# Performance work log

Measured on AMD Instinct MI355X. Metric: run time of the kernel, lower is better.

Reference implementation:

```python
import jax, jax.numpy as jnp
import numpy as np

# ---- static config ----
H, W = 60, 60
WS = 7          # window size (square)
SS = 3          # shift size
DIM = 256
NH = 8
HD = DIM // NH
N = WS * WS     # tokens per window = 49
HP = (H // WS + 1) * WS  # 63 (padded, matches __init__ mask construction)
WP = (W // WS + 1) * WS  # 63
NW = (HP // WS) * (WP // WS)  # 81 windows
EPS = 1e-5


def _rel_pos_index():
    coords = np.stack(np.meshgrid(np.arange(WS), np.arange(WS), indexing='ij'))  # (2,WS,WS)
    cf = coords.reshape(2, -1)                      # (2, N)
    rel = cf[:, :, None] - cf[:, None, :]           # (2, N, N)
    rel = rel.transpose(1, 2, 0).astype(np.int64)   # (N, N, 2)
    rel[..., 0] += WS - 1
    rel[..., 1] += WS - 1
    rel[..., 0] *= 2 * WS - 1
    return rel.sum(-1)                              # (N, N) in [0, 169)


def _attn_mask():
    img = np.zeros((HP, WP), dtype=np.float32)
    cnt = 0
    for hs in (slice(0, -WS), slice(-WS, -SS), slice(-SS, None)):
        for ws_ in (slice(0, -WS), slice(-WS, -SS), slice(-SS, None)):
            img[hs, ws_] = cnt
            cnt += 1
    mw = img.reshape(HP // WS, WS, WP // WS, WS).transpose(0, 2, 1, 3).reshape(-1, N)  # (NW, N)
    diff = mw[:, None, :] - mw[:, :, None]          # (NW, N, N)
    return np.where(diff != 0, -100.0, 0.0).astype(np.float32)


REL_IDX = _rel_pos_index()
ATTN_MASK = _attn_mask()


def layer_norm(x, g, b):
    mu = jnp.mean(x, axis=-1, keepdims=True)
    var = jnp.mean(jnp.square(x - mu), axis=-1, keepdims=True)
    return (x - mu) * jax.lax.rsqrt(var + EPS) * g + b


def setup_inputs() -> dict:
    key = jax.random.key(0)
    ks = jax.random.split(key, 8)
    B = 24
    std = 0.02
    return {
        'x': jax.random.normal(ks[0], (B, H * W, DIM), jnp.float32),
        'g1': jnp.ones((DIM,), jnp.float32),
        'b1': jnp.zeros((DIM,), jnp.float32),
        'w_qkv': jax.random.normal(ks[1], (DIM, 3 * DIM), jnp.float32) * std,
        'b_qkv': jnp.zeros((3 * DIM,), jnp.float32),
        'rel_bias_table': jax.random.normal(ks[2], ((2 * WS - 1) ** 2, NH), jnp.float32) * std,
        'w_proj': jax.random.normal(ks[3], (DIM, DIM), jnp.float32) * std,
        'b_proj': jnp.zeros((DIM,), jnp.float32),
        'g2': jnp.ones((DIM,), jnp.float32),
        'b2': jnp.zeros((DIM,), jnp.float32),
        'w_fc1': jax.random.normal(ks[4], (DIM, 4 * DIM), jnp.float32) * std,
        'b_fc1': jnp.zeros((4 * DIM,), jnp.float32),
        'w_fc2': jax.random.normal(ks[5], (4 * DIM, DIM), jnp.float32) * std,
        'b_fc2': jnp.zeros((DIM,), jnp.float32),
    }


def _swin_block(x, g1, b1, w_qkv, b_qkv, rel_bias_table, w_proj, b_proj,
                g2, b2, w_fc1, b_fc1, w_fc2, b_fc2):
    B, L, C = x.shape
    shortcut = x
    x = layer_norm(x, g1, b1).reshape(B, H, W, C)
    # pad to (HP, WP)
    x = jnp.pad(x, ((0, 0), (0, HP - H), (0, WP - W), (0, 0)))
    # cyclic shift
    x = jnp.roll(x, (-SS, -SS), axis=(1, 2))
    # window partition -> (B*NW, N, C)
    xw = x.reshape(B, HP // WS, WS, WP // WS, WS, C).transpose(0, 1, 3, 2, 4, 5)
    xw = xw.reshape(B * NW, N, C)
    # attention
    qkv = (xw @ w_qkv + b_qkv).reshape(B * NW, N, 3, NH, HD).transpose(2, 0, 3, 1, 4)
    q, k, v = qkv[0], qkv[1], qkv[2]            # (B*NW, NH, N, HD)
    q = q * (HD ** -0.5)
    attn = jnp.einsum('whnd,whmd->whnm', q, k)  # (B*NW, NH, N, N)
    rel_bias = rel_bias_table[jnp.asarray(REL_IDX)]          # (N, N, NH)
    attn = attn + rel_bias.transpose(2, 0, 1)[None]
    mask = jnp.asarray(ATTN_MASK)                            # (NW, N, N)
    attn = attn.reshape(B, NW, NH, N, N) + mask[None, :, None]
    attn = jax.nn.softmax(attn.reshape(B * NW, NH, N, N), axis=-1)
    out = jnp.einsum('whnm,whmd->whnd', attn, v)             # (B*NW, NH, N, HD)
    out = out.transpose(0, 2, 1, 3).reshape(B * NW, N, C)
    out = out @ w_proj + b_proj
    # window reverse -> (B, HP, WP, C)
    out = out.reshape(B, HP // WS, WP // WS, WS, WS, C).transpose(0, 1, 3, 2, 4, 5)
    out = out.reshape(B, HP, WP, C)
    # reverse shift, unpad
    out = jnp.roll(out, (SS, SS), axis=(1, 2))[:, :H, :W, :].reshape(B, L, C)
    x = shortcut + out
    # MLP
    y = layer_norm(x, g2, b2)
    y = jax.nn.gelu(y @ w_fc1 + b_fc1, approximate=False) @ w_fc2 + b_fc2
    return x + y


def reference(x, g1, b1, w_qkv, b_qkv, rel_bias_table, w_proj, b_proj,
              g2, b2, w_fc1, b_fc1, w_fc2, b_fc2):
    return _swin_block(x, g1, b1, w_qkv, b_qkv, rel_bias_table, w_proj, b_proj,
                       g2, b2, w_fc1, b_fc1, w_fc2, b_fc2)
```

## Files before the change

### kernel.cpp

```cpp
#include <hip/hip_runtime.h>
#include <hip/hip_bf16.h>
#include <math.h>


typedef _Float16 half8 __attribute__((ext_vector_type(8)));
typedef _Float16 half4_t __attribute__((ext_vector_type(4)));
typedef float f32x4 __attribute__((ext_vector_type(4)));

#define GLDS16(gp, lp)                                                    \
  __builtin_amdgcn_global_load_lds(                                      \
      (__attribute__((address_space(1))) const void*)(gp),               \
      (__attribute__((address_space(3))) void*)(lp), 16, 0, 0)

__device__ __forceinline__ float wave_reduce_sum(float v) {
  v += __shfl_xor(v, 1);
  v += __shfl_xor(v, 2);
  v += __shfl_xor(v, 4);
  v += __shfl_xor(v, 8);
  v += __shfl_xor(v, 16);
  v += __shfl_xor(v, 32);
  return v;
}

__global__ __launch_bounds__(256) void prep_weights(
    const float* __restrict__ wqkv, const float* __restrict__ wproj,
    const float* __restrict__ wfc1, const float* __restrict__ wfc2,
    _Float16* __restrict__ oqkv, _Float16* __restrict__ oproj,
    _Float16* __restrict__ ofc1, _Float16* __restrict__ ofc2)
{
  int idx = blockIdx.x * 256 + threadIdx.x;
  if (idx < 196608) {
    int n = idx / 256, k = idx % 256;
    oqkv[idx] = (_Float16)wqkv[k * 768 + n];
  } else if (idx < 262144) {
    int i = idx - 196608; int n = i / 256, k = i % 256;
    oproj[i] = (_Float16)wproj[k * 256 + n];
  } else if (idx < 524288) {
    int i = idx - 262144; int n = i / 256, k = i % 256;
    ofc1[i] = (_Float16)wfc1[k * 1024 + n];
  } else {
    int i = idx - 524288; int n = i / 1024, k = i % 1024;
    ofc2[i] = (_Float16)wfc2[k * 256 + n];
  }
}

__global__ __launch_bounds__(256) void prep_cb(
    const float* __restrict__ rbt, _Float16* __restrict__ cbt)
{
  int idx = blockIdx.x * 256 + threadIdx.x;
  int m = idx & 63, n = (idx >> 6) & 63;
  int hc = idx >> 12; int h = hc & 7, c = hc >> 3;
  float v;
  if (n < 49 && m < 49) {
    int i1 = n / 7, j1 = n % 7, i2 = m / 7, j2 = m % 7;
    float bias = rbt[((i1 - i2 + 6) * 13 + (j1 - j2 + 6)) * 8 + h];
    int rh1 = (c & 2) ? (i1 < 4 ? 1 : 2) : 0;
    int rh2 = (c & 2) ? (i2 < 4 ? 1 : 2) : 0;
    int rw1 = (c & 1) ? (j1 < 4 ? 1 : 2) : 0;
    int rw2 = (c & 1) ? (j2 < 4 ? 1 : 2) : 0;
    v = bias + (((rh1 != rh2) || (rw1 != rw2)) ? -100.f : 0.f);
  } else {
    v = -60000.f;
  }
  cbt[idx] = (_Float16)v;
}

__global__ __launch_bounds__(256) void ln1_window_kernel(
    const float* __restrict__ x, const float* __restrict__ g,
    const float* __restrict__ bta, _Float16* __restrict__ xw,
    int row0, int rows_c)
{
  int lrow = blockIdx.x * 4 + (threadIdx.x >> 6);
  if (lrow >= rows_c) return;
  int row = row0 + lrow;
  int lane = threadIdx.x & 63;
  int bw = row / 49, n = row - bw * 49;
  int b = bw / 81, win = bw - b * 81;
  int wh = win / 9, ww = win - wh * 9;
  int i = n / 7, j = n - i * 7;
  int sh = wh * 7 + i + 3; if (sh >= 63) sh -= 63;
  int sw = ww * 7 + j + 3; if (sw >= 63) sw -= 63;
  bool valid = (sh < 60) && (sw < 60);
  float4 v = make_float4(0.f, 0.f, 0.f, 0.f);
  if (valid)
    v = reinterpret_cast<const float4*>(x + ((size_t)b * 3600 + sh * 60 + sw) * 256)[lane];
  float s = v.x + v.y + v.z + v.w;
  s = wave_reduce_sum(s);
  float mu = s * (1.f / 256.f);
  float dx = v.x - mu, dy = v.y - mu, dz = v.z - mu, dw = v.w - mu;
  float q = dx * dx + dy * dy + dz * dz + dw * dw;
  q = wave_reduce_sum(q);
  float rs = rsqrtf(q * (1.f / 256.f) + 1e-5f);
  float4 gv = reinterpret_cast<const float4*>(g)[lane];
  float4 bv = reinterpret_cast<const float4*>(bta)[lane];
  union { _Float16 h[4]; uint2 u; } pk;
  if (valid) {
    pk.h[0] = (_Float16)(dx * rs * gv.x + bv.x);
    pk.h[1] = (_Float16)(dy * rs * gv.y + bv.y);
    pk.h[2] = (_Float16)(dz * rs * gv.z + bv.z);
    pk.h[3] = (_Float16)(dw * rs * gv.w + bv.w);
  } else {
    pk.h[0] = pk.h[1] = pk.h[2] = pk.h[3] = (_Float16)0.f;
  }
  *reinterpret_cast<uint2*>(xw + (size_t)lrow * 256 + lane * 4) = pk.u;
}

__global__ __launch_bounds__(256) void ln2_kernel(
    const float* __restrict__ xin, const float* __restrict__ g,
    const float* __restrict__ bta, _Float16* __restrict__ y)
{
  int row = blockIdx.x * 4 + (threadIdx.x >> 6);
  int lane = threadIdx.x & 63;
  float4 v = reinterpret_cast<const float4*>(xin + (size_t)row * 256)[lane];
  float s = v.x + v.y + v.z + v.w;
  s = wave_reduce_sum(s);
  float mu = s * (1.f / 256.f);
  float dx = v.x - mu, dy = v.y - mu, dz = v.z - mu, dw = v.w - mu;
  float q = dx * dx + dy * dy + dz * dz + dw * dw;
  q = wave_reduce_sum(q);
  float rs = rsqrtf(q * (1.f / 256.f) + 1e-5f);
  float4 gv = reinterpret_cast<const float4*>(g)[lane];
  float4 bv = reinterpret_cast<const float4*>(bta)[lane];
  union { _Float16 h[4]; uint2 u; } pk;
  pk.h[0] = (_Float16)(dx * rs * gv.x + bv.x);
  pk.h[1] = (_Float16)(dy * rs * gv.y + bv.y);
  pk.h[2] = (_Float16)(dz * rs * gv.z + bv.z);
  pk.h[3] = (_Float16)(dw * rs * gv.w + bv.w);
  *reinterpret_cast<uint2*>(y + (size_t)row * 256 + lane * 4) = pk.u;
}

__global__ __launch_bounds__(256, 2) void gemm_kernel(
    const _Float16* __restrict__ A, const _Float16* __restrict__ Bt,
    const float* __restrict__ bias, const float* __restrict__ resid,
    void* __restrict__ out, int M, int N, int K, int mode, int row0)
{
  __shared__ __align__(16) _Float16 lds[2][2][8192];
  const int tid = threadIdx.x;
  const int n0 = blockIdx.x * 128, m0 = blockIdx.y * 128;
  const int wv = tid >> 6, ln = tid & 63;
  const int wm = (wv >> 1) * 64, wn = (wv & 1) * 64;
  const int quad = ln >> 4, l16 = ln & 15;

  const int rl = ln >> 3;
  const int gseg = ((ln & 7) ^ rl) << 3;
  const _Float16* gA[4]; const _Float16* gB[4];
#pragma unroll
  for (int s = 0; s < 4; s++) {
    int r = wv * 32 + s * 8 + rl;
    int gm = m0 + r; if (gm >= M) gm = M - 1;
    gA[s] = A + (size_t)gm * K + gseg;
    gB[s] = Bt + (size_t)(n0 + r) * K + gseg;
  }

  int offA[2][4], offB[2][4];
#pragma unroll
  for (int i = 0; i < 4; i++) {
    int ra = wm + i * 16 + l16;
    int rb = wn + i * 16 + l16;
    int sw0 = l16 & 7;
#pragma unroll
    for (int ks = 0; ks < 2; ks++) {
      offA[ks][i] = ra * 64 + (((ks * 4 + quad) ^ sw0) << 3);
      offB[ks][i] = rb * 64 + (((ks * 4 + quad) ^ sw0) << 3);
    }
  }

  f32x4 acc[4][4];
#pragma unroll
  for (int i = 0; i < 4; i++)
#pragma unroll
    for (int j = 0; j < 4; j++) acc[i][j] = (f32x4)0.f;

#define STAGE(buf, koff)                                                   \
  {                                                                        \
    _Float16* la = &lds[buf][0][wv * 2048];                                \
    _Float16* lb = &lds[buf][1][wv * 2048];                                \
    GLDS16(gA[0] + (koff), la);        GLDS16(gB[0] + (koff), lb);         \
    GLDS16(gA[1] + (koff), la + 512);  GLDS16(gB[1] + (koff), lb + 512);   \
    GLDS16(gA[2] + (koff), la + 1024); GLDS16(gB[2] + (koff), lb + 1024);  \
    GLDS16(gA[3] + (koff), la + 1536); GLDS16(gB[3] + (koff), lb + 1536);  \
  }

  const int nt = K >> 6;
  STAGE(0, 0);
  __syncthreads();
  for (int t = 0; t < nt; t++) {
    const int cur = t & 1;
    half8 a0[4], b0[4], a1[4], b1[4];
#pragma unroll
    for (int i = 0; i < 4; i++) {
      a0[i] = *reinterpret_cast<const half8*>(&lds[cur][0][offA[0][i]]);
      a1[i] = *reinterpret_cast<const half8*>(&lds[cur][0][offA[1][i]]);
      b0[i] = *reinterpret_cast<const half8*>(&lds[cur][1][offB[0][i]]);
      b1[i] = *reinterpret_cast<const half8*>(&lds[cur][1][offB[1][i]]);
    }
    if (t + 1 < nt) STAGE(cur ^ 1, (t + 1) << 6);
#pragma unroll
    for (int i = 0; i < 4; i++)
#pragma unroll
      for (int j = 0; j < 4; j++)
        acc[i][j] = __builtin_amdgcn_mfma_f32_16x16x32_f16(b0[j], a0[i], acc[i][j], 0, 0, 0);
#pragma unroll
    for (int i = 0; i < 4; i++)
#pragma unroll
      for (int j = 0; j < 4; j++)
        acc[i][j] = __builtin_amdgcn_mfma_f32_16x16x32_f16(b1[j], a1[i], acc[i][j], 0, 0, 0);
    __syncthreads();
  }
#undef STAGE

  f32x4 bias4[4];
#pragma unroll
  for (int j = 0; j < 4; j++)
    bias4[j] = *reinterpret_cast<const f32x4*>(bias + n0 + wn + j * 16 + quad * 4);

#pragma unroll
  for (int i = 0; i < 4; i++) {
    int gm = m0 + wm + i * 16 + l16;
    if (gm >= M) continue;
    if (mode == 0) {
      _Float16* op = reinterpret_cast<_Float16*>(out) + (size_t)gm * N + n0 + wn;
#pragma unroll
      for (int j = 0; j < 4; j++) {
        float sc = (n0 + wn + j * 16) < 256 ? 0.17677669529663687f : 1.f;
        half4_t o4;
#pragma unroll
        for (int r = 0; r < 4; r++)
          o4[r] = (_Float16)((acc[i][j][r] + bias4[j][r]) * sc);
        *reinterpret_cast<half4_t*>(op + j * 16 + quad * 4) = o4;
      }
    } else if (mode == 2) {
      _Float16* op = reinterpret_cast<_Float16*>(out) + (size_t)gm * N + n0 + wn;
#pragma unroll
      for (int j = 0; j < 4; j++) {
        half4_t o4;
#pragma unroll
        for (int r = 0; r < 4; r++) {
          float v = acc[i][j][r] + bias4[j][r];
          v = 0.5f * v * (1.f + erff(v * 0.70710678118654752f));
          o4[r] = (_Float16)v;
        }
        *reinterpret_cast<half4_t*>(op + j * 16 + quad * 4) = o4;
      }
    } else if (mode == 3) {
      float* op = reinterpret_cast<float*>(out) + (size_t)gm * N + n0 + wn;
      const float* rp = resid + (size_t)gm * N + n0 + wn;
#pragma unroll
      for (int j = 0; j < 4; j++) {
        f32x4 rv = *reinterpret_cast<const f32x4*>(rp + j * 16 + quad * 4);
        f32x4 v = acc[i][j] + bias4[j] + rv;
        *reinterpret_cast<f32x4*>(op + j * 16 + quad * 4) = v;
      }
    } else {
      int gmg = gm + row0;
      int bw = gmg / 49, nn = gmg - bw * 49;
      int bidx = bw / 81, win = bw - bidx * 81;
      int wh = win / 9, wwn = win - wh * 9;
      int ii = nn / 7, jj = nn - ii * 7;
      int sh = wh * 7 + ii + 3; if (sh >= 63) sh -= 63;
      int sw = wwn * 7 + jj + 3; if (sw >= 63) sw -= 63;
      if (sh < 60 && sw < 60) {
        size_t o = ((size_t)bidx * 3600 + sh * 60 + sw) * 256 + n0 + wn;
        float* op = reinterpret_cast<float*>(out) + o;
        const float* rp = resid + o;
#pragma unroll
        for (int j = 0; j < 4; j++) {
          f32x4 rv = *reinterpret_cast<const f32x4*>(rp + j * 16 + quad * 4);
          f32x4 v = acc[i][j] + bias4[j] + rv;
          *reinterpret_cast<f32x4*>(op + j * 16 + quad * 4) = v;
        }
      }
    }
  }
}

__global__ __launch_bounds__(64) void attn_mfma(
    const _Float16* __restrict__ qkv, const _Float16* __restrict__ cbt,
    _Float16* __restrict__ outp)
{
  __shared__ __align__(16) _Float16 VT[32][72];
  __shared__ __align__(16) _Float16 Ps[64][72];
  const int bwh = blockIdx.x;
  const int bw = bwh >> 3, h = bwh & 7;
  const int win = bw % 81;
  const int wh = win / 9, ww = win - wh * 9;
  const int cls = ((wh == 8) ? 2 : 0) | ((ww == 8) ? 1 : 0);
  const int lane = threadIdx.x;
  const int quad = lane >> 4, l16 = lane & 15;

  for (int e = lane; e < 480; e += 64) {
    int d = e / 15, m = 49 + e % 15;
    VT[d][m] = (_Float16)0.f;
  }
  const size_t vbase = (size_t)bw * 49 * 768 + 512 + h * 32;
  for (int e = lane; e < 1568; e += 64) {
    int m = e >> 5, d = e & 31;
    VT[d][m] = qkv[vbase + (size_t)m * 768 + d];
  }

  const _Float16* qb = qkv + (size_t)bw * 49 * 768 + h * 32 + quad * 8;
  half8 kf[4], qf[4];
  const half8 hz = (half8)(_Float16)0.f;
#pragma unroll
  for (int t = 0; t < 4; t++) {
    int row = t * 16 + l16;
    int rc = row < 49 ? row : 48;
    half8 kv = *reinterpret_cast<const half8*>(qb + 256 + (size_t)rc * 768);
    half8 qv = *reinterpret_cast<const half8*>(qb + (size_t)rc * 768);
    kf[t] = row < 49 ? kv : hz;
    qf[t] = row < 49 ? qv : hz;
  }

  f32x4 S[4][4];
#pragma unroll
  for (int mt = 0; mt < 4; mt++)
#pragma unroll
    for (int nt = 0; nt < 4; nt++) S[mt][nt] = (f32x4)0.f;
#pragma unroll
  for (int mt = 0; mt < 4; mt++)
#pragma unroll
    for (int nt = 0; nt < 4; nt++)
      S[mt][nt] = __builtin_amdgcn_mfma_f32_16x16x32_f16(kf[mt], qf[nt], S[mt][nt], 0, 0, 0);

  const _Float16* cbp = cbt + (((size_t)cls * 8 + h) << 12);
#pragma unroll
  for (int nt = 0; nt < 4; nt++) {
    int n = nt * 16 + l16;
#pragma unroll
    for (int mt = 0; mt < 4; mt++) {
      half4_t cb4 = *reinterpret_cast<const half4_t*>(cbp + n * 64 + mt * 16 + quad * 4);
#pragma unroll
      for (int r = 0; r < 4; r++) S[mt][nt][r] += (float)cb4[r];
    }
  }

  float inv[4];
#pragma unroll
  for (int nt = 0; nt < 4; nt++) {
    float mx = -3.0e38f;
#pragma unroll
    for (int mt = 0; mt < 4; mt++)
#pragma unroll
      for (int r = 0; r < 4; r++) mx = fmaxf(mx, S[mt][nt][r]);
    mx = fmaxf(mx, __shfl_xor(mx, 16));
    mx = fmaxf(mx, __shfl_xor(mx, 32));
    float sm = 0.f;
#pragma unroll
    for (int mt = 0; mt < 4; mt++)
#pragma unroll
      for (int r = 0; r < 4; r++) {
        float e = __expf(S[mt][nt][r] - mx);
        S[mt][nt][r] = e;
        sm += e;
      }
    sm += __shfl_xor(sm, 16);
    sm += __shfl_xor(sm, 32);
    inv[nt] = 1.f / sm;
  }

#pragma unroll
  for (int nt = 0; nt < 4; nt++) {
#pragma unroll
    for (int mt = 0; mt < 4; mt++) {
      half4_t p;
#pragma unroll
      for (int r = 0; r < 4; r++) p[r] = (_Float16)(S[mt][nt][r] * inv[nt]);
      *reinterpret_cast<half4_t*>(&Ps[nt * 16 + l16][mt * 16 + quad * 4]) = p;
    }
  }
  __syncthreads();

  f32x4 O[2][4];
#pragma unroll
  for (int dt = 0; dt < 2; dt++)
#pragma unroll
    for (int nt = 0; nt < 4; nt++) O[dt][nt] = (f32x4)0.f;
#pragma unroll
  for (int ks = 0; ks < 2; ks++) {
    half8 va[2], pb[4];
#pragma unroll
    for (int dt = 0; dt < 2; dt++)
      va[dt] = *reinterpret_cast<const half8*>(&VT[dt * 16 + l16][ks * 32 + quad * 8]);
#pragma unroll
    for (int nt = 0; nt < 4; nt++)
      pb[nt] = *reinterpret_cast<const half8*>(&Ps[nt * 16 + l16][ks * 32 + quad * 8]);
#pragma unroll
    for (int dt = 0; dt < 2; dt++)
#pragma unroll
      for (int nt = 0; nt < 4; nt++)
        O[dt][nt] = __builtin_amdgcn_mfma_f32_16x16x32_f16(va[dt], pb[nt], O[dt][nt], 0, 0, 0);
  }

#pragma unroll
  for (int nt = 0; nt < 4; nt++) {
    int n = nt * 16 + l16;
    if (n < 49) {
#pragma unroll
      for (int dt = 0; dt < 2; dt++) {
        half4_t o4;
#pragma unroll
        for (int r = 0; r < 4; r++) o4[r] = (_Float16)O[dt][nt][r];
        *reinterpret_cast<half4_t*>(
            outp + ((size_t)bw * 49 + n) * 256 + h * 32 + dt * 16 + quad * 4) = o4;
      }
    }
  }
}

extern "C" void kernel_launch(void* const* d_in, const int* in_sizes, int n_in,
                              void* d_out, int out_size, void* d_ws, size_t ws_size,
                              hipStream_t stream) {
  const float* x      = (const float*)d_in[0];
  const float* g1     = (const float*)d_in[1];
  const float* b1     = (const float*)d_in[2];
  const float* w_qkv  = (const float*)d_in[3];
  const float* b_qkv  = (const float*)d_in[4];
  const float* rbt    = (const float*)d_in[5];
  const float* w_proj = (const float*)d_in[6];
  const float* b_proj = (const float*)d_in[7];
  const float* g2     = (const float*)d_in[8];
  const float* b2     = (const float*)d_in[9];
  const float* w_fc1  = (const float*)d_in[10];
  const float* b_fc1  = (const float*)d_in[11];
  const float* w_fc2  = (const float*)d_in[12];
  const float* b_fc2  = (const float*)d_in[13];
  float* outp = (float*)d_out;

  char* ws = (char*)d_ws;
  _Float16* wqkvT  = (_Float16*)(ws + 0);
  _Float16* wprojT = (_Float16*)(ws + 393216);
  _Float16* wfc1T  = (_Float16*)(ws + 524288);
  _Float16* wfc2T  = (_Float16*)(ws + 1048576);
  _Float16* cbt    = (_Float16*)(ws + 1572864);
  const size_t WB = 1835008;

  const int cand[8] = {24, 12, 8, 6, 4, 3, 2, 1};
  int cb = 1;
  for (int ci = 0; ci < 8; ci++) {
    size_t need = WB + (size_t)cand[ci] * (2032128u + 7372800u);
    if (ws_size >= need) { cb = cand[ci]; break; }
  }
  const int nch = 24 / cb;

  _Float16* r1 = (_Float16*)(ws + WB);
  _Float16* r2 = (_Float16*)(ws + WB + (size_t)cb * 2032128u);

  prep_weights<<<3072, 256, 0, stream>>>(w_qkv, w_proj, w_fc1, w_fc2,
                                         wqkvT, wprojT, wfc1T, wfc2T);
  prep_cb<<<512, 256, 0, stream>>>(rbt, cbt);

  for (int c = 0; c < nch; c++) {
    const int b0 = c * cb;
    const int rows_att = cb * 81 * 49;
    const int row0_att = b0 * 81 * 49;
    const int rows_mlp = cb * 3600;
    const int row0_mlp = b0 * 3600;

    ln1_window_kernel<<<(rows_att + 3) / 4, 256, 0, stream>>>(
        x, g1, b1, r1, row0_att, rows_att);
    {
      dim3 g(6, (rows_att + 127) / 128);
      gemm_kernel<<<g, 256, 0, stream>>>(r1, wqkvT, b_qkv, nullptr, r2,
                                         rows_att, 768, 256, 0, 0);
    }
    attn_mfma<<<cb * 81 * 8, 64, 0, stream>>>(r2, cbt, r1);
    {
      dim3 g(2, (rows_att + 127) / 128);
      gemm_kernel<<<g, 256, 0, stream>>>(r1, wprojT, b_proj, x, outp,
                                         rows_att, 256, 256, 1, row0_att);
    }
    ln2_kernel<<<rows_mlp / 4, 256, 0, stream>>>(
        outp + (size_t)row0_mlp * 256, g2, b2, r1);
    {
      dim3 g(8, (rows_mlp + 127) / 128);
      gemm_kernel<<<g, 256, 0, stream>>>(r1, wfc1T, b_fc1, nullptr, r2,
                                         rows_mlp, 1024, 256, 2, 0);
    }
    {
      dim3 g(2, (rows_mlp + 127) / 128);
      float* od = outp + (size_t)row0_mlp * 256;
      gemm_kernel<<<g, 256, 0, stream>>>(r2, wfc2T, b_fc2, od, od,
                                         rows_mlp, 256, 1024, 3, 0);
    }
  }
}
```

Before: 626.1 us.

## Fuse LN2, FC1+GELU and FC2+residual into a single MLP kernel

Replaces the separate LN2 kernel and two MLP GEMM launches with one kernel per 128-row tile. The tile is normalized into LDS, each 128-wide chunk of the hidden activation is computed and kept in LDS after GELU, and it is immediately multiplied into an fp32 accumulator that starts from the residual plus fc2 bias. This removes the global round trips for the LN output and the 1024-wide hidden activation. In exchange it uses large LDS and many registers (occupancy 1), reads weights straight from global without LDS staging, and launches only about 675 blocks per full-batch chunk.

```diff
diff --git a/kernel.cpp b/kernel.cpp
--- a/kernel.cpp
+++ b/kernel.cpp
@@ -105,30 +105,6 @@
   *reinterpret_cast<uint2*>(xw + (size_t)lrow * 256 + lane * 4) = pk.u;
 }
 
-__global__ __launch_bounds__(256) void ln2_kernel(
-    const float* __restrict__ xin, const float* __restrict__ g,
-    const float* __restrict__ bta, _Float16* __restrict__ y)
-{
-  int row = blockIdx.x * 4 + (threadIdx.x >> 6);
-  int lane = threadIdx.x & 63;
-  float4 v = reinterpret_cast<const float4*>(xin + (size_t)row * 256)[lane];
-  float s = v.x + v.y + v.z + v.w;
-  s = wave_reduce_sum(s);
-  float mu = s * (1.f / 256.f);
-  float dx = v.x - mu, dy = v.y - mu, dz = v.z - mu, dw = v.w - mu;
-  float q = dx * dx + dy * dy + dz * dz + dw * dw;
-  q = wave_reduce_sum(q);
-  float rs = rsqrtf(q * (1.f / 256.f) + 1e-5f);
-  float4 gv = reinterpret_cast<const float4*>(g)[lane];
-  float4 bv = reinterpret_cast<const float4*>(bta)[lane];
-  union { _Float16 h[4]; uint2 u; } pk;
-  pk.h[0] = (_Float16)(dx * rs * gv.x + bv.x);
-  pk.h[1] = (_Float16)(dy * rs * gv.y + bv.y);
-  pk.h[2] = (_Float16)(dz * rs * gv.z + bv.z);
-  pk.h[3] = (_Float16)(dw * rs * gv.w + bv.w);
-  *reinterpret_cast<uint2*>(y + (size_t)row * 256 + lane * 4) = pk.u;
-}
-
 __global__ __launch_bounds__(256, 2) void gemm_kernel(
     const _Float16* __restrict__ A, const _Float16* __restrict__ Bt,
     const float* __restrict__ bias, const float* __restrict__ resid,
@@ -228,28 +204,6 @@
         for (int r = 0; r < 4; r++)
           o4[r] = (_Float16)((acc[i][j][r] + bias4[j][r]) * sc);
         *reinterpret_cast<half4_t*>(op + j * 16 + quad * 4) = o4;
-      }
-    } else if (mode == 2) {
-      _Float16* op = reinterpret_cast<_Float16*>(out) + (size_t)gm * N + n0 + wn;
-#pragma unroll
-      for (int j = 0; j < 4; j++) {
-        half4_t o4;
-#pragma unroll
-        for (int r = 0; r < 4; r++) {
-          float v = acc[i][j][r] + bias4[j][r];
-          v = 0.5f * v * (1.f + erff(v * 0.70710678118654752f));
-          o4[r] = (_Float16)v;
-        }
-        *reinterpret_cast<half4_t*>(op + j * 16 + quad * 4) = o4;
-      }
-    } else if (mode == 3) {
-      float* op = reinterpret_cast<float*>(out) + (size_t)gm * N + n0 + wn;
-      const float* rp = resid + (size_t)gm * N + n0 + wn;
-#pragma unroll
-      for (int j = 0; j < 4; j++) {
-        f32x4 rv = *reinterpret_cast<const f32x4*>(rp + j * 16 + quad * 4);
-        f32x4 v = acc[i][j] + bias4[j] + rv;
-        *reinterpret_cast<f32x4*>(op + j * 16 + quad * 4) = v;
       }
     } else {
       int gmg = gm + row0;
@@ -271,6 +225,149 @@
         }
       }
     }
+  }
+}
+
+__global__ __launch_bounds__(256, 1) void fused_mlp_kernel(
+    const float* __restrict__ X, const _Float16* __restrict__ W1t,
+    const float* __restrict__ B1v, const _Float16* __restrict__ W2t,
+    const float* __restrict__ B2v, const float* __restrict__ g,
+    const float* __restrict__ bt, float* __restrict__ out, int M)
+{
+  __shared__ __align__(16) _Float16 Alds[128 * 256];
+  __shared__ __align__(16) _Float16 Hlds[128 * 128];
+  const int tid = threadIdx.x;
+  const int wv = tid >> 6, ln = tid & 63;
+  const int quad = ln >> 4, l16 = ln & 15;
+  const int m0 = blockIdx.x * 128;
+  const int wm = (wv >> 1) * 64;
+  const int wn = (wv & 1) * 64;
+  const int wn2 = (wv & 1) * 128;
+
+  {
+    float4 gv = reinterpret_cast<const float4*>(g)[ln];
+    float4 bv = reinterpret_cast<const float4*>(bt)[ln];
+    int seg = ln >> 1;
+    for (int rr = 0; rr < 32; rr++) {
+      int lr = wv * 32 + rr;
+      int gr = m0 + lr; if (gr >= M) gr = M - 1;
+      float4 v = reinterpret_cast<const float4*>(X + (size_t)gr * 256)[ln];
+      float s = wave_reduce_sum(v.x + v.y + v.z + v.w);
+      float mu = s * (1.f / 256.f);
+      float dx = v.x - mu, dy = v.y - mu, dz = v.z - mu, dw = v.w - mu;
+      float q = wave_reduce_sum(dx * dx + dy * dy + dz * dz + dw * dw);
+      float rs = rsqrtf(q * (1.f / 256.f) + 1e-5f);
+      union { _Float16 h[4]; uint2 u; } pk;
+      pk.h[0] = (_Float16)(dx * rs * gv.x + bv.x);
+      pk.h[1] = (_Float16)(dy * rs * gv.y + bv.y);
+      pk.h[2] = (_Float16)(dz * rs * gv.z + bv.z);
+      pk.h[3] = (_Float16)(dw * rs * gv.w + bv.w);
+      *reinterpret_cast<uint2*>(
+          &Alds[lr * 256 + ((seg ^ (lr & 31)) << 3) + (ln & 1) * 4]) = pk.u;
+    }
+  }
+
+  f32x4 acc[4][8];
+  {
+    f32x4 b2q[8];
+#pragma unroll
+    for (int j = 0; j < 8; j++)
+      b2q[j] = *reinterpret_cast<const f32x4*>(B2v + wn2 + j * 16 + quad * 4);
+#pragma unroll
+    for (int i = 0; i < 4; i++) {
+      int gr = m0 + wm + i * 16 + l16; if (gr >= M) gr = M - 1;
+      const float* xp = X + (size_t)gr * 256 + wn2;
+#pragma unroll
+      for (int j = 0; j < 8; j++)
+        acc[i][j] = *reinterpret_cast<const f32x4*>(xp + j * 16 + quad * 4) + b2q[j];
+    }
+  }
+  __syncthreads();
+
+  for (int n1 = 0; n1 < 8; n1++) {
+    f32x4 acch[4][4];
+#pragma unroll
+    for (int i = 0; i < 4; i++)
+#pragma unroll
+      for (int j = 0; j < 4; j++) acch[i][j] = (f32x4)0.f;
+    for (int t = 0; t < 4; t++) {
+#pragma unroll
+      for (int ks = 0; ks < 2; ks++) {
+        half8 bf[4], af[4];
+#pragma unroll
+        for (int j = 0; j < 4; j++)
+          bf[j] = *reinterpret_cast<const half8*>(
+              W1t + (size_t)(n1 * 128 + wn + j * 16 + l16) * 256 + t * 64 + ks * 32 + quad * 8);
+#pragma unroll
+        for (int i = 0; i < 4; i++) {
+          int ra = wm + i * 16 + l16;
+          af[i] = *reinterpret_cast<const half8*>(
+              &Alds[ra * 256 + (((t * 8 + ks * 4 + quad) ^ (ra & 31)) << 3)]);
+        }
+#pragma unroll
+        for (int i = 0; i < 4; i++)
+#pragma unroll
+          for (int j = 0; j < 4; j++)
+            acch[i][j] = __builtin_amdgcn_mfma_f32_16x16x32_f16(bf[j], af[i], acch[i][j], 0, 0, 0);
+      }
+    }
+    __syncthreads();
+    {
+      f32x4 b1q[4];
+#pragma unroll
+      for (int j = 0; j < 4; j++)
+        b1q[j] = *reinterpret_cast<const f32x4*>(B1v + n1 * 128 + wn + j * 16 + quad * 4);
+#pragma unroll
+      for (int i = 0; i < 4; i++) {
+        int mrow = wm + i * 16 + l16;
+#pragma unroll
+        for (int j = 0; j < 4; j++) {
+          int c = wn + j * 16 + quad * 4;
+          half4_t o4;
+#pragma unroll
+          for (int r = 0; r < 4; r++) {
+            float v = acch[i][j][r] + b1q[j][r];
+            v = 0.5f * v * (1.f + erff(v * 0.70710678118654752f));
+            o4[r] = (_Float16)v;
+          }
+          *reinterpret_cast<half4_t*>(
+              &Hlds[mrow * 128 + (((c >> 3) ^ (mrow & 15)) << 3) + (quad & 1) * 4]) = o4;
+        }
+      }
+    }
+    __syncthreads();
+#pragma unroll
+    for (int t2 = 0; t2 < 2; t2++) {
+#pragma unroll
+      for (int ks = 0; ks < 2; ks++) {
+        half8 hf[4], b2f[8];
+#pragma unroll
+        for (int i = 0; i < 4; i++) {
+          int mh = wm + i * 16 + l16;
+          hf[i] = *reinterpret_cast<const half8*>(
+              &Hlds[mh * 128 + (((t2 * 8 + ks * 4 + quad) ^ (mh & 15)) << 3)]);
+        }
+#pragma unroll
+        for (int j = 0; j < 8; j++)
+          b2f[j] = *reinterpret_cast<const half8*>(
+              W2t + (size_t)(wn2 + j * 16 + l16) * 1024 + n1 * 128 + t2 * 64 + ks * 32 + quad * 8);
+#pragma unroll
+        for (int i = 0; i < 4; i++)
+#pragma unroll
+          for (int j = 0; j < 8; j++)
+            acc[i][j] = __builtin_amdgcn_mfma_f32_16x16x32_f16(b2f[j], hf[i], acc[i][j], 0, 0, 0);
+      }
+    }
+  }
+
+#pragma unroll
+  for (int i = 0; i < 4; i++) {
+    int gm = m0 + wm + i * 16 + l16;
+    if (gm >= M) continue;
+    float* op = out + (size_t)gm * 256 + wn2;
+#pragma unroll
+    for (int j = 0; j < 8; j++)
+      *reinterpret_cast<f32x4*>(op + j * 16 + quad * 4) = acc[i][j];
   }
 }
 
@@ -437,7 +534,7 @@
   const int cand[8] = {24, 12, 8, 6, 4, 3, 2, 1};
   int cb = 1;
   for (int ci = 0; ci < 8; ci++) {
-    size_t need = WB + (size_t)cand[ci] * (2032128u + 7372800u);
+    size_t need = WB + (size_t)cand[ci] * (2032128u + 6096384u);
     if (ws_size >= need) { cb = cand[ci]; break; }
   }
   const int nch = 24 / cb;
@@ -469,18 +566,10 @@
       gemm_kernel<<<g, 256, 0, stream>>>(r1, wprojT, b_proj, x, outp,
                                          rows_att, 256, 256, 1, row0_att);
     }
-    ln2_kernel<<<rows_mlp / 4, 256, 0, stream>>>(
-        outp + (size_t)row0_mlp * 256, g2, b2, r1);
     {
-      dim3 g(8, (rows_mlp + 127) / 128);
-      gemm_kernel<<<g, 256, 0, stream>>>(r1, wfc1T, b_fc1, nullptr, r2,
-                                         rows_mlp, 1024, 256, 2, 0);
-    }
-    {
-      dim3 g(2, (rows_mlp + 127) / 128);
       float* od = outp + (size_t)row0_mlp * 256;
-      gemm_kernel<<<g, 256, 0, stream>>>(r2, wfc2T, b_fc2, od, od,
-                                         rows_mlp, 256, 1024, 3, 0);
-    }
-  }
-}
+      fused_mlp_kernel<<<(rows_mlp + 127) / 128, 256, 0, stream>>>(
+          od, wfc1T, b_fc1, wfc2T, b_fc2, g2, b2, od, rows_mlp);
+    }
+  }
+}
```

Result: slower. 753.9 us (+20.4%).
